# Performance work log

Measured on AMD Instinct MI355X. Metric: run time of the kernel, lower is better.

## Reference

```python
import jax, jax.numpy as jnp
import numpy as np

N_NODES = 100000
N_EDGES = 800000
IN_DIM = 128
HID = 16
HEADS1 = 8
HEADS2 = 10
OUT_DIM = 10
NEG_SLOPE = 0.2  # PyG GATConv default


def segment_softmax(logits, seg, num_segments):
    # logits: [E, H], seg: [E] destination node ids
    m = jax.ops.segment_max(logits, seg, num_segments=num_segments)  # [N, H]
    m = jnp.where(jnp.isfinite(m), m, 0.0)
    e = jnp.exp(logits - m[seg])
    s = jax.ops.segment_sum(e, seg, num_segments=num_segments)  # [N, H]
    return e / (s[seg] + 1e-16)


def gat_conv(x, src, dst, W, a_src, a_dst, bias, heads, out_ch, concat):
    N = x.shape[0]
    h = (x @ W).reshape(N, heads, out_ch)  # [N, H, C]
    alpha_src = jnp.einsum('nhc,hc->nh', h, a_src)
    alpha_dst = jnp.einsum('nhc,hc->nh', h, a_dst)
    logits = jax.nn.leaky_relu(alpha_src[src] + alpha_dst[dst], NEG_SLOPE)  # [E, H]
    alpha = segment_softmax(logits, dst, N)  # [E, H]
    msg = h[src] * alpha[:, :, None]  # [E, H, C]
    out = jax.ops.segment_sum(msg, dst, num_segments=N)  # [N, H, C]
    out = out.reshape(N, heads * out_ch) if concat else out.mean(axis=1)
    return out + bias


def setup_inputs() -> dict:
    key = jax.random.key(0)
    ks = jax.random.split(key, 12)
    g = 0.1
    return {
        'x': jax.random.normal(ks[0], (N_NODES, IN_DIM), jnp.float32),
        'edge_index': jax.random.randint(ks[1], (2, N_EDGES), 0, N_NODES, jnp.int64),
        'labels': jax.random.randint(ks[2], (N_NODES,), 0, OUT_DIM, jnp.int64),
        'train_mask': jax.random.randint(ks[3], (N_NODES,), 0, 2, jnp.int32).astype(bool),
        'W1': jax.random.normal(ks[4], (IN_DIM, HEADS1 * HID), jnp.float32) * g,
        'a_src1': jax.random.normal(ks[5], (HEADS1, HID), jnp.float32) * g,
        'a_dst1': jax.random.normal(ks[6], (HEADS1, HID), jnp.float32) * g,
        'b1': jnp.zeros((HEADS1 * HID,), jnp.float32),
        'W2': jax.random.normal(ks[7], (HEADS1 * HID, HEADS2 * OUT_DIM), jnp.float32) * g,
        'a_src2': jax.random.normal(ks[8], (HEADS2, OUT_DIM), jnp.float32) * g,
        'a_dst2': jax.random.normal(ks[9], (HEADS2, OUT_DIM), jnp.float32) * g,
        'b2': jnp.zeros((OUT_DIM,), jnp.float32),
    }


def reference(x, edge_index, labels, train_mask, W1, a_src1, a_dst1, b1, W2, a_src2, a_dst2, b2):
    # dropout layers are identity in eval mode
    src, dst = edge_index[0], edge_index[1]
    emb1 = gat_conv(x, src, dst, W1, a_src1, a_dst1, b1, HEADS1, HID, concat=True)   # [N, H1*HID]
    h = jax.nn.elu(emb1)
    emb2 = gat_conv(h, src, dst, W2, a_src2, a_dst2, b2, HEADS2, OUT_DIM, concat=False)  # [N, OUT]
    logp = jax.nn.log_softmax(emb2, axis=-1)
    ce = -jnp.take_along_axis(logp, labels[:, None], axis=-1)[:, 0]  # [N]
    m = train_mask.astype(emb2.dtype)
    loss = jnp.sum(ce * m) / jnp.sum(m)
    return (loss, emb1, emb2)
```

## Files before the change

kernel.cpp:

```cpp
#include <hip/hip_runtime.h>
#include <hip/hip_bf16.h>
#include <math.h>

#define N_NODES 100000
#define N_EDGES 800000
#define NB_SCAN ((N_NODES + 1023) / 1024)

typedef __bf16 bf16x8 __attribute__((ext_vector_type(8)));
typedef float  f32x4  __attribute__((ext_vector_type(4)));

__device__ __forceinline__ float lrelu(float v){ return v > 0.f ? v : 0.2f*v; }
__device__ __forceinline__ float eluf(float v){ return v > 0.f ? v : (__expf(v) - 1.f); }

__device__ __forceinline__ unsigned short f2bf(float f){
    union { float f; unsigned u; } v; v.f = f;
    unsigned r = (v.u + 0x7fff + ((v.u >> 16) & 1)) >> 16;
    return (unsigned short)r;
}
__device__ __forceinline__ float bf2f(unsigned short u){
    union { unsigned u; float f; } v; v.u = ((unsigned)u) << 16;
    return v.f;
}

__global__ __launch_bounds__(256) void setup_kernel(
    const float* __restrict__ W1, const float* __restrict__ W2,
    unsigned short* __restrict__ wt1, unsigned short* __restrict__ wt2,
    int* __restrict__ counts, float* __restrict__ lacc)
{
    int i = blockIdx.x*256 + threadIdx.x;
    if (i < N_NODES) counts[i] = 0;
    if (i < 4) lacc[i] = 0.f;
    if (i < 128*128){
        int n = i >> 7, k = i & 127;
        wt1[i] = f2bf(W1[k*128 + n]);
    }
    if (i < 112*128){
        int n = i >> 7, k = i & 127;
        wt2[i] = (n < 100) ? f2bf(W2[k*100 + n]) : (unsigned short)0;
    }
}

__global__ __launch_bounds__(256) void count_kernel(const int* __restrict__ ei,
                                                    int* __restrict__ counts,
                                                    int* __restrict__ rank){
    int e = blockIdx.x*256 + threadIdx.x;
    if (e < N_EDGES){
        int d = ei[N_EDGES + e];
        rank[e] = atomicAdd(&counts[d], 1);
    }
}

__global__ __launch_bounds__(1024) void scan_blocks_kernel(const int* __restrict__ counts,
                                                           int* __restrict__ exoffs,
                                                           int* __restrict__ bsums){
    __shared__ int buf[1024];
    int t = threadIdx.x;
    int gid = blockIdx.x*1024 + t;
    int v = (gid < N_NODES) ? counts[gid] : 0;
    buf[t] = v;
    __syncthreads();
    #pragma unroll
    for (int off = 1; off < 1024; off <<= 1){
        int u = (t >= off) ? buf[t-off] : 0;
        __syncthreads();
        buf[t] += u;
        __syncthreads();
    }
    if (gid < N_NODES) exoffs[gid] = buf[t] - v;
    if (t == 1023) bsums[blockIdx.x] = buf[1023];
}

__global__ void scan_sums_kernel(const int* __restrict__ bsums, int* __restrict__ bpre){
    if (threadIdx.x == 0){
        int run = 0;
        #pragma unroll 4
        for (int b = 0; b < NB_SCAN; b++){ int v = bsums[b]; bpre[b] = run; run += v; }
    }
}

__global__ __launch_bounds__(1024) void scan_add_kernel(const int* __restrict__ exoffs,
                                                        const int* __restrict__ bpre,
                                                        int* __restrict__ offs){
    int gid = blockIdx.x*1024 + threadIdx.x;
    if (gid < N_NODES){
        offs[gid] = exoffs[gid] + bpre[blockIdx.x];
    }
    if (gid == 0) offs[N_NODES] = N_EDGES;
}

__global__ __launch_bounds__(256) void scatter_kernel(
    const int* __restrict__ ei, const int* __restrict__ offs, const int* __restrict__ rank,
    int* __restrict__ csr_src, int* __restrict__ csr_dst)
{
    int e = blockIdx.x*256 + threadIdx.x;
    if (e >= N_EDGES) return;
    int s = ei[e];
    int d = ei[N_EDGES + e];
    int slot = offs[d] + rank[e];
    csr_src[slot] = s;
    csr_dst[slot] = d;
}

__global__ __launch_bounds__(256) void wk1_kernel(
    const int* __restrict__ csr_src, const int* __restrict__ csr_dst,
    const float* __restrict__ as1, const float* __restrict__ ad1,
    unsigned short* __restrict__ w1bf)
{
    int e = blockIdx.x*256 + threadIdx.x;
    if (e >= N_EDGES) return;
    int s = csr_src[e];
    int d = csr_dst[e];
    const f32x4* ap = (const f32x4*)(as1 + s*8);
    const f32x4* dp = (const f32x4*)(ad1 + d*8);
    f32x4 a0 = ap[0], a1 = ap[1];
    f32x4 d0 = dp[0], d1 = dp[1];
    ushort4 o0, o1;
    o0.x = f2bf(__expf(lrelu(a0[0]+d0[0])));
    o0.y = f2bf(__expf(lrelu(a0[1]+d0[1])));
    o0.z = f2bf(__expf(lrelu(a0[2]+d0[2])));
    o0.w = f2bf(__expf(lrelu(a0[3]+d0[3])));
    o1.x = f2bf(__expf(lrelu(a1[0]+d1[0])));
    o1.y = f2bf(__expf(lrelu(a1[1]+d1[1])));
    o1.z = f2bf(__expf(lrelu(a1[2]+d1[2])));
    o1.w = f2bf(__expf(lrelu(a1[3]+d1[3])));
    *(ushort4*)&w1bf[(size_t)e*8]     = o0;
    *(ushort4*)&w1bf[(size_t)e*8 + 4] = o1;
}

__global__ __launch_bounds__(256) void wk2_kernel(
    const int* __restrict__ csr_src, const int* __restrict__ csr_dst,
    const float* __restrict__ as2, const float* __restrict__ ad2,
    unsigned short* __restrict__ w2bf)
{
    int e = blockIdx.x*256 + threadIdx.x;
    if (e >= N_EDGES) return;
    int s = csr_src[e];
    int d = csr_dst[e];
    const float* ap = as2 + s*10;
    const float* dp = ad2 + d*10;
    unsigned short o[10];
    #pragma unroll
    for (int h = 0; h < 10; h++) o[h] = f2bf(__expf(lrelu(ap[h] + dp[h])));
    ushort2* wp = (ushort2*)&w2bf[(size_t)e*10];
    #pragma unroll
    for (int h = 0; h < 5; h++) wp[h] = make_ushort2(o[2*h], o[2*h+1]);
}

__global__ __launch_bounds__(256) void gemm1_mfma(
    const float* __restrict__ x, const unsigned short* __restrict__ wt1,
    const float* __restrict__ a_src, const float* __restrict__ a_dst,
    unsigned short* __restrict__ h1bf, float* __restrict__ as1, float* __restrict__ ad1)
{
    __shared__ unsigned short Al[32*128];
    __shared__ unsigned short Bl[128*128];
    int t = threadIdx.x;
    int row0 = blockIdx.x*32;

    #pragma unroll
    for (int i = 0; i < 2; i++){
        int idx = (i*256 + t)*8;
        int r = idx >> 7, c = idx & 127;
        int grow = row0 + r;
        bf16x8 v;
        if (grow < N_NODES){
            const float4* p = (const float4*)(x + (size_t)grow*128 + c);
            float4 f0 = p[0], f1 = p[1];
            v[0]=(__bf16)f0.x; v[1]=(__bf16)f0.y; v[2]=(__bf16)f0.z; v[3]=(__bf16)f0.w;
            v[4]=(__bf16)f1.x; v[5]=(__bf16)f1.y; v[6]=(__bf16)f1.z; v[7]=(__bf16)f1.w;
        } else {
            #pragma unroll
            for (int j = 0; j < 8; j++) v[j] = (__bf16)0.f;
        }
        int byte = (r*256 + c*2) ^ ((r&7)<<4);
        *(bf16x8*)((char*)Al + byte) = v;
    }
    #pragma unroll
    for (int i = 0; i < 8; i++){
        int idx = (i*256 + t)*8;
        int n = idx >> 7, c = idx & 127;
        bf16x8 v = *(const bf16x8*)(wt1 + n*128 + c);
        int byte = (n*256 + c*2) ^ ((n&7)<<4);
        *(bf16x8*)((char*)Bl + byte) = v;
    }
    __syncthreads();

    int wv = t >> 6, l = t & 63;
    int wm = wv >> 1, wn = wv & 1;
    int lr = l & 15, lg = l >> 4;
    bf16x8 af[4];
    #pragma unroll
    for (int ks = 0; ks < 4; ks++){
        int r = wm*16 + lr;
        int byte = (r*256 + (ks*32 + lg*8)*2) ^ ((r&7)<<4);
        af[ks] = *(const bf16x8*)((const char*)Al + byte);
    }
    f32x4 acc[4];
    #pragma unroll
    for (int nt = 0; nt < 4; nt++){
        acc[nt] = (f32x4){0.f,0.f,0.f,0.f};
        #pragma unroll
        for (int ks = 0; ks < 4; ks++){
            int n = wn*64 + nt*16 + lr;
            int byte = (n*256 + (ks*32 + lg*8)*2) ^ ((n&7)<<4);
            bf16x8 bfv = *(const bf16x8*)((const char*)Bl + byte);
            acc[nt] = __builtin_amdgcn_mfma_f32_16x16x32_bf16(af[ks], bfv, acc[nt], 0, 0, 0);
        }
    }
    int orow_base = row0 + wm*16 + lg*4;
    #pragma unroll
    for (int nt = 0; nt < 4; nt++){
        int colb = wn*64 + nt*16;
        int head = colb >> 4;
        float avs = a_src[colb + lr];
        float avd = a_dst[colb + lr];
        #pragma unroll
        for (int r = 0; r < 4; r++){
            int grow = orow_base + r;
            float v = acc[nt][r];
            if (grow < N_NODES) h1bf[(size_t)grow*128 + colb + lr] = f2bf(v);
            float ps = v*avs, pd = v*avd;
            ps += __shfl_xor(ps,1); ps += __shfl_xor(ps,2); ps += __shfl_xor(ps,4); ps += __shfl_xor(ps,8);
            pd += __shfl_xor(pd,1); pd += __shfl_xor(pd,2); pd += __shfl_xor(pd,4); pd += __shfl_xor(pd,8);
            if (lr == 0 && grow < N_NODES){
                as1[grow*8 + head] = ps;
                ad1[grow*8 + head] = pd;
            }
        }
    }
}

__global__ __launch_bounds__(256) void agg1_kernel(
    const int* __restrict__ offs, const int* __restrict__ csr_src,
    const unsigned short* __restrict__ w1bf,
    const unsigned short* __restrict__ h1bf, const float* __restrict__ b1,
    float* __restrict__ emb1_out )
{
    int wave = threadIdx.x >> 6;
    int lane = threadIdx.x & 63;
    int d = blockIdx.x*4 + wave;
    if (d >= N_NODES) return;
    int h = lane >> 3;
    int col = 2*lane;
    int e0 = offs[d], e1 = offs[d+1];
    float acc0 = 0.f, acc1 = 0.f, wsum = 0.f;

    for (int base = e0; base < e1; base += 64){
        int ii = base + lane;
        int sv = (ii < e1) ? csr_src[ii] : 0;
        int n = min(64, e1 - base);
        for (int i = 0; i < n; i += 8){
            const unsigned short* wp = w1bf + (size_t)(base + i)*8 + h;
            int sj[8]; unsigned hj[8];
            #pragma unroll
            for (int j = 0; j < 8; j++) sj[j] = __shfl(sv, i+j);
            #pragma unroll
            for (int j = 0; j < 8; j++) hj[j] = *(const unsigned*)(h1bf + (size_t)sj[j]*128 + col);
            #pragma unroll
            for (int j = 0; j < 8; j++){
                float w = bf2f(wp[j*8]);
                w = (i + j < n) ? w : 0.f;
                acc0 += w*bf2f((unsigned short)hj[j]);
                acc1 += w*bf2f((unsigned short)(hj[j]>>16));
                wsum += w;
            }
        }
    }
    float inv = 1.f/(wsum + 1e-16f);
    emb1_out[(size_t)d*128 + col]     = acc0*inv + b1[col];
    emb1_out[(size_t)d*128 + col + 1] = acc1*inv + b1[col+1];
}

__global__ __launch_bounds__(256) void gemm2_mfma(
    const float* __restrict__ emb1g , const unsigned short* __restrict__ wt2,
    const float* __restrict__ a_src2, const float* __restrict__ a_dst2,
    unsigned short* __restrict__ h2bf, float* __restrict__ as2, float* __restrict__ ad2)
{
    __shared__ __align__(16) char smem[36864];
    unsigned short* Al = (unsigned short*)smem;
    unsigned short* Bl = Al + 32*128;
    float* Hl = (float*)smem;

    int t = threadIdx.x;
    int row0 = blockIdx.x*32;

    #pragma unroll
    for (int i = 0; i < 2; i++){
        int idx = (i*256 + t)*8;
        int r = idx >> 7, c = idx & 127;
        int grow = row0 + r;
        bf16x8 v;
        if (grow < N_NODES){
            const float4* p = (const float4*)(emb1g + (size_t)grow*128 + c);
            float4 f0 = p[0], f1 = p[1];
            v[0]=(__bf16)eluf(f0.x); v[1]=(__bf16)eluf(f0.y); v[2]=(__bf16)eluf(f0.z); v[3]=(__bf16)eluf(f0.w);
            v[4]=(__bf16)eluf(f1.x); v[5]=(__bf16)eluf(f1.y); v[6]=(__bf16)eluf(f1.z); v[7]=(__bf16)eluf(f1.w);
        } else {
            #pragma unroll
            for (int j = 0; j < 8; j++) v[j] = (__bf16)0.f;
        }
        int byte = (r*256 + c*2) ^ ((r&7)<<4);
        *(bf16x8*)((char*)Al + byte) = v;
    }
    #pragma unroll
    for (int i = 0; i < 7; i++){
        int idx = (i*256 + t)*8;
        int n = idx >> 7, c = idx & 127;
        bf16x8 v = *(const bf16x8*)(wt2 + n*128 + c);
        int byte = (n*256 + c*2) ^ ((n&7)<<4);
        *(bf16x8*)((char*)Bl + byte) = v;
    }
    __syncthreads();

    int wv = t >> 6, l = t & 63;
    int wm = wv >> 1, wn = wv & 1;
    int lr = l & 15, lg = l >> 4;
    bf16x8 af[4];
    #pragma unroll
    for (int ks = 0; ks < 4; ks++){
        int r = wm*16 + lr;
        int byte = (r*256 + (ks*32 + lg*8)*2) ^ ((r&7)<<4);
        af[ks] = *(const bf16x8*)((const char*)Al + byte);
    }
    int ntmax = wn ? 3 : 4;
    f32x4 acc[4];
    for (int nt = 0; nt < ntmax; nt++){
        acc[nt] = (f32x4){0.f,0.f,0.f,0.f};
        #pragma unroll
        for (int ks = 0; ks < 4; ks++){
            int n = wn*64 + nt*16 + lr;
            int byte = (n*256 + (ks*32 + lg*8)*2) ^ ((n&7)<<4);
            bf16x8 bfv = *(const bf16x8*)((const char*)Bl + byte);
            acc[nt] = __builtin_amdgcn_mfma_f32_16x16x32_bf16(af[ks], bfv, acc[nt], 0, 0, 0);
        }
    }
    int orow_base = row0 + wm*16 + lg*4;
    for (int nt = 0; nt < ntmax; nt++){
        int col = wn*64 + nt*16 + lr;
        if (col < 100){
            #pragma unroll
            for (int r = 0; r < 4; r++){
                int grow = orow_base + r;
                if (grow < N_NODES) h2bf[(size_t)grow*100 + col] = f2bf(acc[nt][r]);
            }
        }
    }
    __syncthreads();
    for (int nt = 0; nt < ntmax; nt++){
        int col = wn*64 + nt*16 + lr;
        int rbase = wm*16 + lg*4;
        #pragma unroll
        for (int r = 0; r < 4; r++) Hl[(rbase + r)*113 + col] = acc[nt][r];
    }
    __syncthreads();
    for (int task = t; task < 320; task += 256){
        int row = task/10, h = task - row*10;
        int grow = row0 + row;
        if (grow < N_NODES){
            const float* p = &Hl[row*113 + h*10];
            float s = 0.f, dd = 0.f;
            #pragma unroll
            for (int c = 0; c < 10; c++){
                float v = p[c];
                s  += v*a_src2[h*10 + c];
                dd += v*a_dst2[h*10 + c];
            }
            as2[grow*10 + h] = s;
            ad2[grow*10 + h] = dd;
        }
    }
}

__global__ __launch_bounds__(256) void agg2_kernel(
    const int* __restrict__ offs, const int* __restrict__ csr_src,
    const unsigned short* __restrict__ w2bf,
    const unsigned short* __restrict__ h2bf, const float* __restrict__ b2,
    float* __restrict__ emb2_out)
{
    __shared__ float sval[4][100];
    int wv = threadIdx.x >> 6;
    int lane = threadIdx.x & 63;
    int d = blockIdx.x*4 + wv;
    if (d >= N_NODES) return;
    int c0 = 2*lane;
    bool act = lane < 50;
    int h = lane/5; if (h > 9) h = 9;
    int e0 = offs[d], e1 = offs[d+1];
    float acc0 = 0.f, acc1 = 0.f, wsum = 0.f;

    for (int base = e0; base < e1; base += 64){
        int ii = base + lane;
        int sv = (ii < e1) ? csr_src[ii] : 0;
        int n = min(64, e1 - base);
        for (int i = 0; i < n; i += 8){
            const unsigned short* wp = w2bf + (size_t)(base + i)*10 + h;
            int sj[8]; unsigned vj[8];
            #pragma unroll
            for (int j = 0; j < 8; j++) sj[j] = __shfl(sv, i+j);
            #pragma unroll
            for (int j = 0; j < 8; j++) vj[j] = act ? *(const unsigned*)(h2bf + (size_t)sj[j]*100 + c0) : 0u;
            #pragma unroll
            for (int j = 0; j < 8; j++){
                float w = bf2f(wp[j*10]);
                w = (i + j < n) ? w : 0.f;
                acc0 += w*bf2f((unsigned short)vj[j]);
                acc1 += w*bf2f((unsigned short)(vj[j]>>16));
                wsum += w;
            }
        }
    }
    if (act){
        float inv = 1.f/(wsum + 1e-16f);
        sval[wv][c0]   = acc0*inv;
        sval[wv][c0+1] = acc1*inv;
    }
    __syncthreads();
    if (lane < 10){
        float s = 0.f;
        #pragma unroll
        for (int hh = 0; hh < 10; hh++) s += sval[wv][hh*10 + lane];
        emb2_out[(size_t)d*10 + lane] = s*0.1f + b2[lane];
    }
}

__global__ __launch_bounds__(256) void loss_kernel(
    const float* __restrict__ emb2, const int* __restrict__ labels,
    const int* __restrict__ mask, float* __restrict__ acc)
{
    int i = blockIdx.x*256 + threadIdx.x;
    float num = 0.f, den = 0.f;
    if (i < N_NODES && mask[i] != 0){
        const float* v = emb2 + (size_t)i*10;
        float m = v[0];
        #pragma unroll
        for (int c = 1; c < 10; c++) m = fmaxf(m, v[c]);
        float s = 0.f;
        #pragma unroll
        for (int c = 0; c < 10; c++) s += __expf(v[c]-m);
        float lse = m + __logf(s);
        num = lse - v[labels[i]];
        den = 1.f;
    }
    #pragma unroll
    for (int o = 32; o >= 1; o >>= 1){ num += __shfl_down(num, o); den += __shfl_down(den, o); }
    if ((threadIdx.x & 63) == 0){
        atomicAdd(&acc[0], num);
        atomicAdd(&acc[1], den);
    }
}

__global__ void finalize_kernel(const float* __restrict__ acc, float* __restrict__ out0){
    out0[0] = acc[0]/acc[1];
}

extern "C" void kernel_launch(void* const* d_in, const int* in_sizes, int n_in,
                              void* d_out, int out_size, void* d_ws, size_t ws_size,
                              hipStream_t stream) {
    const float* x      = (const float*)d_in[0];
    const int*   ei     = (const int*)d_in[1];
    const int*   labels = (const int*)d_in[2];
    const int*   mask   = (const int*)d_in[3];
    const float* W1     = (const float*)d_in[4];
    const float* a_src1 = (const float*)d_in[5];
    const float* a_dst1 = (const float*)d_in[6];
    const float* b1     = (const float*)d_in[7];
    const float* W2     = (const float*)d_in[8];
    const float* a_src2 = (const float*)d_in[9];
    const float* a_dst2 = (const float*)d_in[10];
    const float* b2     = (const float*)d_in[11];

    float* out  = (float*)d_out;
    float* emb1 = out + 1;
    float* emb2 = out + 1 + (size_t)N_NODES*128;

    unsigned short* h1bf = (unsigned short*)d_ws;
    unsigned short* h2bf = h1bf + (size_t)N_NODES*128;
    unsigned short* w1bf = h2bf + (size_t)N_NODES*100;
    unsigned short* w2bf = w1bf + (size_t)(N_EDGES+8)*8;
    float* as1  = (float*)(w2bf + (size_t)(N_EDGES+8)*10);
    float* ad1  = as1 + (size_t)N_NODES*8;
    float* as2  = ad1 + (size_t)N_NODES*8;
    float* ad2  = as2 + (size_t)N_NODES*10;
    float* lacc = ad2 + (size_t)N_NODES*10;
    int* counts = (int*)(lacc + 4);
    int* offs   = counts + N_NODES;
    int* rank   = offs + N_NODES + 1;
    int* csr    = rank + N_EDGES;
    int* csrd   = csr + N_EDGES;
    int* exoffs = csrd + N_EDGES;
    int* bsums  = exoffs + N_NODES;
    int* bpre   = bsums + NB_SCAN;
    unsigned short* wt1 = (unsigned short*)(bpre + NB_SCAN);
    unsigned short* wt2 = wt1 + 128*128;

    setup_kernel<<<(N_NODES+255)/256, 256, 0, stream>>>(W1, W2, wt1, wt2, counts, lacc);
    count_kernel<<<N_EDGES/256, 256, 0, stream>>>(ei, counts, rank);
    scan_blocks_kernel<<<NB_SCAN, 1024, 0, stream>>>(counts, exoffs, bsums);
    scan_sums_kernel<<<1, 64, 0, stream>>>(bsums, bpre);
    scan_add_kernel<<<NB_SCAN, 1024, 0, stream>>>(exoffs, bpre, offs);
    scatter_kernel<<<N_EDGES/256, 256, 0, stream>>>(ei, offs, rank, csr, csrd);

    int gblocks = (N_NODES + 31)/32;
    gemm1_mfma<<<gblocks, 256, 0, stream>>>(x, wt1, a_src1, a_dst1, h1bf, as1, ad1);
    wk1_kernel<<<N_EDGES/256, 256, 0, stream>>>(csr, csrd, as1, ad1, w1bf);
    agg1_kernel<<<(N_NODES + 3)/4, 256, 0, stream>>>(offs, csr, w1bf, h1bf, b1, emb1);
    gemm2_mfma<<<gblocks, 256, 0, stream>>>(emb1, wt2, a_src2, a_dst2, h2bf, as2, ad2);
    wk2_kernel<<<N_EDGES/256, 256, 0, stream>>>(csr, csrd, as2, ad2, w2bf);
    agg2_kernel<<<(N_NODES + 3)/4, 256, 0, stream>>>(offs, csr, w2bf, h2bf, b2, emb2);
    loss_kernel<<<(N_NODES+255)/256, 256, 0, stream>>>(emb2, labels, mask, lacc);
    finalize_kernel<<<1, 1, 0, stream>>>(lacc, out);
}
```

Measured before the change: 285.0 us.

## Make GEMM kernels persistent so weight tiles load once per block

```diff
diff --git a/kernel.cpp b/kernel.cpp
--- a/kernel.cpp
+++ b/kernel.cpp
@@ -5,6 +5,10 @@
 #define N_NODES 100000
 #define N_EDGES 800000
 #define NB_SCAN ((N_NODES + 1023) / 1024)
+#define GB1 ((N_NODES + 31)/32)
+#define SB  ((N_EDGES + 255)/256)
+#define PG1 1024
+#define PG2 768
 
 typedef __bf16 bf16x8 __attribute__((ext_vector_type(8)));
 typedef float  f32x4  __attribute__((ext_vector_type(4)));
@@ -154,26 +158,7 @@
     __shared__ unsigned short Al[32*128];
     __shared__ unsigned short Bl[128*128];
     int t = threadIdx.x;
-    int row0 = blockIdx.x*32;
-
-    #pragma unroll
-    for (int i = 0; i < 2; i++){
-        int idx = (i*256 + t)*8;
-        int r = idx >> 7, c = idx & 127;
-        int grow = row0 + r;
-        bf16x8 v;
-        if (grow < N_NODES){
-            const float4* p = (const float4*)(x + (size_t)grow*128 + c);
-            float4 f0 = p[0], f1 = p[1];
-            v[0]=(__bf16)f0.x; v[1]=(__bf16)f0.y; v[2]=(__bf16)f0.z; v[3]=(__bf16)f0.w;
-            v[4]=(__bf16)f1.x; v[5]=(__bf16)f1.y; v[6]=(__bf16)f1.z; v[7]=(__bf16)f1.w;
-        } else {
-            #pragma unroll
-            for (int j = 0; j < 8; j++) v[j] = (__bf16)0.f;
-        }
-        int byte = (r*256 + c*2) ^ ((r&7)<<4);
-        *(bf16x8*)((char*)Al + byte) = v;
-    }
+
     #pragma unroll
     for (int i = 0; i < 8; i++){
         int idx = (i*256 + t)*8;
@@ -182,50 +167,74 @@
         int byte = (n*256 + c*2) ^ ((n&7)<<4);
         *(bf16x8*)((char*)Bl + byte) = v;
     }
-    __syncthreads();
 
     int wv = t >> 6, l = t & 63;
     int wm = wv >> 1, wn = wv & 1;
     int lr = l & 15, lg = l >> 4;
-    bf16x8 af[4];
-    #pragma unroll
-    for (int ks = 0; ks < 4; ks++){
-        int r = wm*16 + lr;
-        int byte = (r*256 + (ks*32 + lg*8)*2) ^ ((r&7)<<4);
-        af[ks] = *(const bf16x8*)((const char*)Al + byte);
-    }
-    f32x4 acc[4];
-    #pragma unroll
-    for (int nt = 0; nt < 4; nt++){
-        acc[nt] = (f32x4){0.f,0.f,0.f,0.f};
+
+    for (int tile = blockIdx.x; tile < GB1; tile += PG1){
+        int row0 = tile*32;
+        #pragma unroll
+        for (int i = 0; i < 2; i++){
+            int idx = (i*256 + t)*8;
+            int r = idx >> 7, c = idx & 127;
+            int grow = row0 + r;
+            bf16x8 v;
+            if (grow < N_NODES){
+                const float4* p = (const float4*)(x + (size_t)grow*128 + c);
+                float4 f0 = p[0], f1 = p[1];
+                v[0]=(__bf16)f0.x; v[1]=(__bf16)f0.y; v[2]=(__bf16)f0.z; v[3]=(__bf16)f0.w;
+                v[4]=(__bf16)f1.x; v[5]=(__bf16)f1.y; v[6]=(__bf16)f1.z; v[7]=(__bf16)f1.w;
+            } else {
+                #pragma unroll
+                for (int j = 0; j < 8; j++) v[j] = (__bf16)0.f;
+            }
+            int byte = (r*256 + c*2) ^ ((r&7)<<4);
+            *(bf16x8*)((char*)Al + byte) = v;
+        }
+        __syncthreads();
+
+        bf16x8 af[4];
         #pragma unroll
         for (int ks = 0; ks < 4; ks++){
-            int n = wn*64 + nt*16 + lr;
-            int byte = (n*256 + (ks*32 + lg*8)*2) ^ ((n&7)<<4);
-            bf16x8 bfv = *(const bf16x8*)((const char*)Bl + byte);
-            acc[nt] = __builtin_amdgcn_mfma_f32_16x16x32_bf16(af[ks], bfv, acc[nt], 0, 0, 0);
-        }
-    }
-    int orow_base = row0 + wm*16 + lg*4;
-    #pragma unroll
-    for (int nt = 0; nt < 4; nt++){
-        int colb = wn*64 + nt*16;
-        int head = colb >> 4;
-        float avs = a_src[colb + lr];
-        float avd = a_dst[colb + lr];
-        #pragma unroll
-        for (int r = 0; r < 4; r++){
-            int grow = orow_base + r;
-            float v = acc[nt][r];
-            if (grow < N_NODES) h1bf[(size_t)grow*128 + colb + lr] = f2bf(v);
-            float ps = v*avs, pd = v*avd;
-            ps += __shfl_xor(ps,1); ps += __shfl_xor(ps,2); ps += __shfl_xor(ps,4); ps += __shfl_xor(ps,8);
-            pd += __shfl_xor(pd,1); pd += __shfl_xor(pd,2); pd += __shfl_xor(pd,4); pd += __shfl_xor(pd,8);
-            if (lr == 0 && grow < N_NODES){
-                as1[grow*8 + head] = ps;
-                ad1[grow*8 + head] = pd;
-            }
-        }
+            int r = wm*16 + lr;
+            int byte = (r*256 + (ks*32 + lg*8)*2) ^ ((r&7)<<4);
+            af[ks] = *(const bf16x8*)((const char*)Al + byte);
+        }
+        f32x4 acc[4];
+        #pragma unroll
+        for (int nt = 0; nt < 4; nt++){
+            acc[nt] = (f32x4){0.f,0.f,0.f,0.f};
+            #pragma unroll
+            for (int ks = 0; ks < 4; ks++){
+                int n = wn*64 + nt*16 + lr;
+                int byte = (n*256 + (ks*32 + lg*8)*2) ^ ((n&7)<<4);
+                bf16x8 bfv = *(const bf16x8*)((const char*)Bl + byte);
+                acc[nt] = __builtin_amdgcn_mfma_f32_16x16x32_bf16(af[ks], bfv, acc[nt], 0, 0, 0);
+            }
+        }
+        int orow_base = row0 + wm*16 + lg*4;
+        #pragma unroll
+        for (int nt = 0; nt < 4; nt++){
+            int colb = wn*64 + nt*16;
+            int head = colb >> 4;
+            float avs = a_src[colb + lr];
+            float avd = a_dst[colb + lr];
+            #pragma unroll
+            for (int r = 0; r < 4; r++){
+                int grow = orow_base + r;
+                float v = acc[nt][r];
+                if (grow < N_NODES) h1bf[(size_t)grow*128 + colb + lr] = f2bf(v);
+                float ps = v*avs, pd = v*avd;
+                ps += __shfl_xor(ps,1); ps += __shfl_xor(ps,2); ps += __shfl_xor(ps,4); ps += __shfl_xor(ps,8);
+                pd += __shfl_xor(pd,1); pd += __shfl_xor(pd,2); pd += __shfl_xor(pd,4); pd += __shfl_xor(pd,8);
+                if (lr == 0 && grow < N_NODES){
+                    as1[grow*8 + head] = ps;
+                    ad1[grow*8 + head] = pd;
+                }
+            }
+        }
+        __syncthreads();
     }
 }
 
@@ -275,32 +284,11 @@
     const float* __restrict__ a_src2, const float* __restrict__ a_dst2,
     unsigned short* __restrict__ h2bf, float* __restrict__ as2, float* __restrict__ ad2)
 {
-    __shared__ __align__(16) char smem[36864];
-    unsigned short* Al = (unsigned short*)smem;
-    unsigned short* Bl = Al + 32*128;
-    float* Hl = (float*)smem;
-
+    __shared__ unsigned short Al[32*128];
+    __shared__ unsigned short Bl[112*128];
+    __shared__ float Hl[32*113];
     int t = threadIdx.x;
-    int row0 = blockIdx.x*32;
-
-    #pragma unroll
-    for (int i = 0; i < 2; i++){
-        int idx = (i*256 + t)*8;
-        int r = idx >> 7, c = idx & 127;
-        int grow = row0 + r;
-        bf16x8 v;
-        if (grow < N_NODES){
-            const float4* p = (const float4*)(emb1g + (size_t)grow*128 + c);
-            float4 f0 = p[0], f1 = p[1];
-            v[0]=(__bf16)eluf(f0.x); v[1]=(__bf16)eluf(f0.y); v[2]=(__bf16)eluf(f0.z); v[3]=(__bf16)eluf(f0.w);
-            v[4]=(__bf16)eluf(f1.x); v[5]=(__bf16)eluf(f1.y); v[6]=(__bf16)eluf(f1.z); v[7]=(__bf16)eluf(f1.w);
-        } else {
-            #pragma unroll
-            for (int j = 0; j < 8; j++) v[j] = (__bf16)0.f;
-        }
-        int byte = (r*256 + c*2) ^ ((r&7)<<4);
-        *(bf16x8*)((char*)Al + byte) = v;
-    }
+
     #pragma unroll
     for (int i = 0; i < 7; i++){
         int idx = (i*256 + t)*8;
@@ -309,64 +297,87 @@
         int byte = (n*256 + c*2) ^ ((n&7)<<4);
         *(bf16x8*)((char*)Bl + byte) = v;
     }
-    __syncthreads();
 
     int wv = t >> 6, l = t & 63;
     int wm = wv >> 1, wn = wv & 1;
     int lr = l & 15, lg = l >> 4;
-    bf16x8 af[4];
-    #pragma unroll
-    for (int ks = 0; ks < 4; ks++){
-        int r = wm*16 + lr;
-        int byte = (r*256 + (ks*32 + lg*8)*2) ^ ((r&7)<<4);
-        af[ks] = *(const bf16x8*)((const char*)Al + byte);
-    }
     int ntmax = wn ? 3 : 4;
-    f32x4 acc[4];
-    for (int nt = 0; nt < ntmax; nt++){
-        acc[nt] = (f32x4){0.f,0.f,0.f,0.f};
+
+    for (int tile = blockIdx.x; tile < GB1; tile += PG2){
+        int row0 = tile*32;
+        #pragma unroll
+        for (int i = 0; i < 2; i++){
+            int idx = (i*256 + t)*8;
+            int r = idx >> 7, c = idx & 127;
+            int grow = row0 + r;
+            bf16x8 v;
+            if (grow < N_NODES){
+                const float4* p = (const float4*)(emb1g + (size_t)grow*128 + c);
+                float4 f0 = p[0], f1 = p[1];
+                v[0]=(__bf16)eluf(f0.x); v[1]=(__bf16)eluf(f0.y); v[2]=(__bf16)eluf(f0.z); v[3]=(__bf16)eluf(f0.w);
+                v[4]=(__bf16)eluf(f1.x); v[5]=(__bf16)eluf(f1.y); v[6]=(__bf16)eluf(f1.z); v[7]=(__bf16)eluf(f1.w);
+            } else {
+                #pragma unroll
+                for (int j = 0; j < 8; j++) v[j] = (__bf16)0.f;
+            }
+            int byte = (r*256 + c*2) ^ ((r&7)<<4);
+            *(bf16x8*)((char*)Al + byte) = v;
+        }
+        __syncthreads();
+
+        bf16x8 af[4];
         #pragma unroll
         for (int ks = 0; ks < 4; ks++){
-            int n = wn*64 + nt*16 + lr;
-            int byte = (n*256 + (ks*32 + lg*8)*2) ^ ((n&7)<<4);
-            bf16x8 bfv = *(const bf16x8*)((const char*)Bl + byte);
-            acc[nt] = __builtin_amdgcn_mfma_f32_16x16x32_bf16(af[ks], bfv, acc[nt], 0, 0, 0);
-        }
-    }
-    int orow_base = row0 + wm*16 + lg*4;
-    for (int nt = 0; nt < ntmax; nt++){
-        int col = wn*64 + nt*16 + lr;
-        if (col < 100){
-            #pragma unroll
-            for (int r = 0; r < 4; r++){
-                int grow = orow_base + r;
-                if (grow < N_NODES) h2bf[(size_t)grow*100 + col] = f2bf(acc[nt][r]);
-            }
-        }
-    }
-    __syncthreads();
-    for (int nt = 0; nt < ntmax; nt++){
-        int col = wn*64 + nt*16 + lr;
-        int rbase = wm*16 + lg*4;
-        #pragma unroll
-        for (int r = 0; r < 4; r++) Hl[(rbase + r)*113 + col] = acc[nt][r];
-    }
-    __syncthreads();
-    for (int task = t; task < 320; task += 256){
-        int row = task/10, h = task - row*10;
-        int grow = row0 + row;
-        if (grow < N_NODES){
-            const float* p = &Hl[row*113 + h*10];
-            float s = 0.f, dd = 0.f;
-            #pragma unroll
-            for (int c = 0; c < 10; c++){
-                float v = p[c];
-                s  += v*a_src2[h*10 + c];
-                dd += v*a_dst2[h*10 + c];
-            }
-            as2[grow*10 + h] = s;
-            ad2[grow*10 + h] = dd;
-        }
+            int r = wm*16 + lr;
+            int byte = (r*256 + (ks*32 + lg*8)*2) ^ ((r&7)<<4);
+            af[ks] = *(const bf16x8*)((const char*)Al + byte);
+        }
+        f32x4 acc[4];
+        for (int nt = 0; nt < ntmax; nt++){
+            acc[nt] = (f32x4){0.f,0.f,0.f,0.f};
+            #pragma unroll
+            for (int ks = 0; ks < 4; ks++){
+                int n = wn*64 + nt*16 + lr;
+                int byte = (n*256 + (ks*32 + lg*8)*2) ^ ((n&7)<<4);
+                bf16x8 bfv = *(const bf16x8*)((const char*)Bl + byte);
+                acc[nt] = __builtin_amdgcn_mfma_f32_16x16x32_bf16(af[ks], bfv, acc[nt], 0, 0, 0);
+            }
+        }
+        int orow_base = row0 + wm*16 + lg*4;
+        for (int nt = 0; nt < ntmax; nt++){
+            int col = wn*64 + nt*16 + lr;
+            if (col < 100){
+                #pragma unroll
+                for (int r = 0; r < 4; r++){
+                    int grow = orow_base + r;
+                    if (grow < N_NODES) h2bf[(size_t)grow*100 + col] = f2bf(acc[nt][r]);
+                }
+            }
+        }
+        for (int nt = 0; nt < ntmax; nt++){
+            int col = wn*64 + nt*16 + lr;
+            int rbase = wm*16 + lg*4;
+            #pragma unroll
+            for (int r = 0; r < 4; r++) Hl[(rbase + r)*113 + col] = acc[nt][r];
+        }
+        __syncthreads();
+        for (int task = t; task < 320; task += 256){
+            int row = task/10, h = task - row*10;
+            int grow = row0 + row;
+            if (grow < N_NODES){
+                const float* p = &Hl[row*113 + h*10];
+                float s = 0.f, dd = 0.f;
+                #pragma unroll
+                for (int c = 0; c < 10; c++){
+                    float v = p[c];
+                    s  += v*a_src2[h*10 + c];
+                    dd += v*a_dst2[h*10 + c];
+                }
+                as2[grow*10 + h] = s;
+                ad2[grow*10 + h] = dd;
+            }
+        }
+        __syncthreads();
     }
 }
 
@@ -493,18 +504,17 @@
     unsigned short* wt2 = wt1 + 128*128;
 
     setup_kernel<<<(N_NODES+255)/256, 256, 0, stream>>>(W1, W2, wt1, wt2, counts, lacc);
-    count_kernel<<<N_EDGES/256, 256, 0, stream>>>(ei, counts, rank);
+    count_kernel<<<SB, 256, 0, stream>>>(ei, counts, rank);
     scan_blocks_kernel<<<NB_SCAN, 1024, 0, stream>>>(counts, exoffs, bsums);
     scan_sums_kernel<<<1, 64, 0, stream>>>(bsums, bpre);
     scan_add_kernel<<<NB_SCAN, 1024, 0, stream>>>(exoffs, bpre, offs);
-    scatter_kernel<<<N_EDGES/256, 256, 0, stream>>>(ei, offs, rank, csr, csrd);
-
-    int gblocks = (N_NODES + 31)/32;
-    gemm1_mfma<<<gblocks, 256, 0, stream>>>(x, wt1, a_src1, a_dst1, h1bf, as1, ad1);
-    wk1_kernel<<<N_EDGES/256, 256, 0, stream>>>(csr, csrd, as1, ad1, w1bf);
+    scatter_kernel<<<SB, 256, 0, stream>>>(ei, offs, rank, csr, csrd);
+
+    gemm1_mfma<<<PG1, 256, 0, stream>>>(x, wt1, a_src1, a_dst1, h1bf, as1, ad1);
+    wk1_kernel<<<SB, 256, 0, stream>>>(csr, csrd, as1, ad1, w1bf);
     agg1_kernel<<<(N_NODES + 3)/4, 256, 0, stream>>>(offs, csr, w1bf, h1bf, b1, emb1);
-    gemm2_mfma<<<gblocks, 256, 0, stream>>>(emb1, wt2, a_src2, a_dst2, h2bf, as2, ad2);
-    wk2_kernel<<<N_EDGES/256, 256, 0, stream>>>(csr, csrd, as2, ad2, w2bf);
+    gemm2_mfma<<<PG2, 256, 0, stream>>>(emb1, wt2, a_src2, a_dst2, h2bf, as2, ad2);
+    wk2_kernel<<<SB, 256, 0, stream>>>(csr, csrd, as2, ad2, w2bf);
     agg2_kernel<<<(N_NODES + 3)/4, 256, 0, stream>>>(offs, csr, w2bf, h2bf, b2, emb2);
     loss_kernel<<<(N_NODES+255)/256, 256, 0, stream>>>(emb2, labels, mask, lacc);
     finalize_kernel<<<1, 1, 0, stream>>>(lacc, out);
```

After: 282.5 us. Within noise of the previous version (-0.9%).
